# Optimization experiments

Hardware: AMD Instinct MI355X
Metric: run time of the kernel (lower is better)

Reference implementation:

```python
import jax, jax.numpy as jnp
import numpy as np

B, C1, C2, K, S, HDIM = 8, 16, 16, 3, 1, 16
H = W = 64


def setup_inputs() -> dict:
    key = jax.random.key(0)
    k0, k1, k2 = jax.random.split(key, 3)
    x = jax.random.normal(k0, (B, C1, H, W), jnp.float32)
    # torch.nn.Linear default init scale ~ 1/sqrt(fan_in)
    fc1_w = jax.random.normal(k1, (HDIM, 5), jnp.float32) * (1.0 / np.sqrt(5.0))
    fc1_b = jnp.zeros((HDIM,), jnp.float32)
    fc2_w = jax.random.normal(k2, (C2 * C1 * K * K, HDIM), jnp.float32) * (1.0 / np.sqrt(HDIM))
    fc2_b = jnp.zeros((C2 * C1 * K * K,), jnp.float32)
    return {"x": x, "fc1_w": fc1_w, "fc1_b": fc1_b, "fc2_w": fc2_w, "fc2_b": fc2_b}


def _unfold_same(x, k, s):
    """F.pad('same'-style) + F.unfold. Returns (patches [B, L, C*k*k], out_h, out_w).
    Channel ordering matches torch unfold: index = c*k*k + i*k + j (channel-major)."""
    Bq, C, Hq, Wq = x.shape
    out_h = (Hq + s - 1) // s
    out_w = (Wq + s - 1) // s
    pad_h = max((out_h - 1) * s + k - Hq, 0)
    pad_w = max((out_w - 1) * s + k - Wq, 0)
    pt, pb = pad_h // 2, pad_h - pad_h // 2
    pl, pr = pad_w // 2, pad_w - pad_w // 2
    xp = jnp.pad(x, ((0, 0), (0, 0), (pt, pb), (pl, pr)))
    # k*k shifted views; loop over tiny fixed k*k=9 taps only
    cols = jnp.stack(
        [xp[:, :, i:i + out_h * s:s, j:j + out_w * s:s] for i in range(k) for j in range(k)],
        axis=2,
    )  # [B, C, k*k, out_h, out_w]
    patches = cols.reshape(Bq, C * k * k, out_h * out_w).transpose(0, 2, 1)  # [B, L, C*k*k]
    return patches, out_h, out_w


def reference(x, fc1_w, fc1_b, fc2_w, fc2_b):
    patches, oh, ow = _unfold_same(x, K, S)  # [B, L, N] with N = C1*K*K
    Bq, L, N = patches.shape
    mu = patches.mean(-1, keepdims=True)
    # torch.std default is unbiased (ddof=1)
    var = jnp.sum((patches - mu) ** 2, axis=-1, keepdims=True) / (N - 1)
    sigma = jnp.sqrt(var) + 1e-6
    normed = (patches - mu) / sigma
    skew = jnp.mean(normed ** 3, axis=-1, keepdims=True)
    kurt = jnp.mean(normed ** 4, axis=-1, keepdims=True) - 3.0
    prob = jax.nn.softmax(patches, axis=-1)
    entropy = -jnp.sum(prob * jnp.log(prob + 1e-6), axis=-1, keepdims=True)
    stats = jnp.concatenate([mu, sigma, skew, kurt, entropy], axis=-1)  # [B, L, 5]
    stats = jax.lax.stop_gradient(stats)  # .detach() in the original
    h = jax.nn.relu(stats @ fc1_w.T + fc1_b)                 # [B, L, hdim]
    weights = (h @ fc2_w.T + fc2_b).reshape(Bq, L, C2, N)    # [B, L, c2, c1*k*k]
    out = jnp.einsum('blco,blo->blc', weights, patches)      # per-location dynamic conv
    return out.transpose(0, 2, 1).reshape(Bq, C2, oh, ow)
```

## Files before the change

### kernel.cpp

```cpp
#include <hip/hip_runtime.h>
#include <math.h>


typedef __attribute__((ext_vector_type(8))) short short8;
typedef __attribute__((ext_vector_type(4))) float float4v;

#define NPq 144
#define QSTR 280

__device__ __forceinline__ unsigned short f2bf(float f) {
    unsigned int u = __builtin_bit_cast(unsigned int, f);
    u += 0x7fffu + ((u >> 16) & 1u);
    return (unsigned short)(u >> 16);
}
__device__ __forceinline__ float bf2f(unsigned short h) {
    unsigned int u = ((unsigned int)h) << 16;
    return __builtin_bit_cast(float, u);
}

__global__ void prep_bfrag(const float* __restrict__ fc2_w,
                           const float* __restrict__ fc2_b,
                           unsigned short* __restrict__ Bfrag) {
    const int blk  = blockIdx.x;
    const int t    = blk / 5, s = blk % 5;
    const int lane = threadIdx.x;
    const int n    = lane & 15, q = lane >> 4;
    short8 v;
#pragma unroll
    for (int j = 0; j < 8; ++j) {
        const int k = s * 32 + q * 8 + j;
        float w = 0.f;
        if (k < NPq) w = (t < 16) ? fc2_w[(t * NPq + k) * 16 + n]
                                  : fc2_b[n * NPq + k];
        v[j] = (short)f2bf(w);
    }
    *(short8*)(Bfrag + (size_t)(blk * 64 + lane) * 8) = v;
}

__global__ __launch_bounds__(256, 2) void sacconv_kernel(
    const float* __restrict__ x,
    const float* __restrict__ fc1_w,
    const float* __restrict__ fc1_b,
    const unsigned short* __restrict__ Bfrag,
    float* __restrict__ out)
{
    __shared__ unsigned short SA[4 * 5 * 64 * 8];
    __shared__ __attribute__((aligned(16))) unsigned short Qs[64 * QSTR];
    __shared__ float Hl[64][20];

    const int t   = threadIdx.x;
    const int blk = blockIdx.x;
    const int b   = blk >> 6;
    const int y   = blk & 63;

    const int lane = t & 63;
    const int w    = __builtin_amdgcn_readfirstlane(t >> 6);
    const int m    = lane & 15;
    const int q    = lane >> 4;
    const int loc  = w * 16 + m;

    float* XsG = (float*)Qs;
    float* Xs  = XsG + 4;

    const short8* Bf = (const short8*)Bfrag;
    short8 bb0[5], bb1[5], bb2[5];
#pragma unroll
    for (int s = 0; s < 5; ++s) bb0[s] = Bf[(w * 5 + s) * 64 + lane];

    {
        const float4 z4 = make_float4(0.f, 0.f, 0.f, 0.f);
        if (t < 48) *(float4*)&Xs[t * 68 + 64] = z4;
        if (t == 48) *(float4*)&XsG[0] = z4;
        const int ybad = (y == 0) ? 0 : ((y == 63) ? 2 : -1);
        if (ybad >= 0) {
#pragma unroll
            for (int u = 0; u < 2; ++u) {
                const int idx = t + 256 * u;
                if (idx < 272) {
                    const int ch = idx / 17, sg = idx % 17;
                    *(float4*)&Xs[ch * 204 + ybad * 68 + sg * 4] = z4;
                }
            }
        }
#pragma unroll
        for (int u = 0; u < 3; ++u) {
            const int idx = t + 256 * u;
            const int r  = idx >> 4, sg = idx & 15;
            const int ch = r / 3;
            const int dy = r - ch * 3;
            const int yy = y + dy - 1;
            if (yy >= 0 && yy < 64) {
                const float4 d = *(const float4*)&x[(((b * 16 + ch) * 64 + yy) << 6) + sg * 4];
                *(float4*)&Xs[r * 68 + sg * 4] = d;
            }
        }
    }
    __syncthreads();

    float v[36];
    float sum = 0.f, mx = -1e30f;
    {
        const float* basep = &Xs[q * 816 + loc - 1];
#pragma unroll
        for (int i = 0; i < 36; ++i) {
            const int g  = i / 9;
            const int r9 = i % 9;
            const int ii = r9 / 3, jj = r9 % 3;
            const float val = basep[g * 204 + ii * 68 + jj];
            v[i] = val;
            sum += val;
            mx  = fmaxf(mx, val);
        }
    }

    {
        unsigned int pk[18];
#pragma unroll
        for (int p = 0; p < 18; ++p)
            pk[p] = (unsigned int)f2bf(v[2 * p]) | ((unsigned int)f2bf(v[2 * p + 1]) << 16);
        const int g0 = (36 * q) >> 3;
        auto hwa = [&](int g) { return ((w * 5 + (g >> 2)) * 64 + (g & 3) * 16 + m) * 8; };
        if ((q & 1) == 0) {
#pragma unroll
            for (int u = 0; u < 4; ++u)
                *(uint4*)&SA[hwa(g0 + u)] = make_uint4(pk[4*u], pk[4*u+1], pk[4*u+2], pk[4*u+3]);
            *(uint2*)&SA[hwa(g0 + 4)] = make_uint2(pk[16], pk[17]);
        } else {
            *(uint2*)&SA[hwa(g0) + 4] = make_uint2(pk[0], pk[1]);
#pragma unroll
            for (int u = 0; u < 4; ++u)
                *(uint4*)&SA[hwa(g0 + 1 + u)] = make_uint4(pk[4*u+2], pk[4*u+3], pk[4*u+4], pk[4*u+5]);
        }
        if (lane < 32)
            *(uint4*)&SA[((w * 5 + 4) * 64 + 32 + lane) * 8] = make_uint4(0u, 0u, 0u, 0u);
    }

    sum += __shfl_xor(sum, 16, 64);
    sum += __shfl_xor(sum, 32, 64);
    mx = fmaxf(mx, __shfl_xor(mx, 16, 64));
    mx = fmaxf(mx, __shfl_xor(mx, 32, 64));
    const float mu = sum * (1.f / 144.f);

    float m2 = 0.f, m3 = 0.f, m4 = 0.f, se = 0.f, sev = 0.f;
#pragma unroll
    for (int i = 0; i < 36; ++i) {
        const float d  = v[i] - mu;
        const float d2 = d * d;
        m2 += d2; m3 += d2 * d; m4 += d2 * d2;
        const float e = __expf(v[i] - mx);
        se += e; sev += e * v[i];
    }
    m2 += __shfl_xor(m2, 16, 64);  m2 += __shfl_xor(m2, 32, 64);
    m3 += __shfl_xor(m3, 16, 64);  m3 += __shfl_xor(m3, 32, 64);
    m4 += __shfl_xor(m4, 16, 64);  m4 += __shfl_xor(m4, 32, 64);
    se += __shfl_xor(se, 16, 64);  se += __shfl_xor(se, 32, 64);
    sev += __shfl_xor(sev, 16, 64); sev += __shfl_xor(sev, 32, 64);

    const float var   = m2 * (1.f / 143.f);
    const float sigma = sqrtf(var) + 1e-6f;
    const float is    = 1.f / sigma;
    const float is2   = is * is;
    const float skew  = (m3 * (1.f / 144.f)) * is2 * is;
    const float kurt  = (m4 * (1.f / 144.f)) * is2 * is2 - 3.f;
    const float ent   = __logf(se) + mx - sev / se;

    {
        float h4[4];
#pragma unroll
        for (int j0 = 0; j0 < 4; ++j0) {
            const int j = q * 4 + j0;
            const float* wr = fc1_w + j * 5;
            const float hv = mu * wr[0] + sigma * wr[1] + skew * wr[2]
                           + kurt * wr[3] + ent * wr[4] + fc1_b[j];
            h4[j0] = fmaxf(hv, 0.f);
        }
        *(float4*)&Hl[loc][q * 4] = make_float4(h4[0], h4[1], h4[2], h4[3]);
    }

#pragma unroll
    for (int s = 0; s < 5; ++s) bb1[s] = Bf[((w + 4) * 5 + s) * 64 + lane];

    __syncthreads();

    short8 af[4][5];
#pragma unroll
    for (int mm = 0; mm < 4; ++mm)
#pragma unroll
        for (int s = 0; s < 5; ++s)
            af[mm][s] = *(const short8*)&SA[((mm * 5 + s) * 64 + lane) * 8];

    float4v acc[4][4];
#pragma unroll
    for (int u = 0; u < 4; ++u)
#pragma unroll
        for (int mm = 0; mm < 4; ++mm) acc[u][mm] = (float4v){0.f, 0.f, 0.f, 0.f};
    float4v acc4[4];
#pragma unroll
    for (int mm = 0; mm < 4; ++mm) acc4[mm] = (float4v){0.f, 0.f, 0.f, 0.f};

#pragma unroll
    for (int s = 0; s < 5; ++s) bb2[s] = Bf[((w + 8) * 5 + s) * 64 + lane];
#pragma unroll
    for (int mm = 0; mm < 4; ++mm)
#pragma unroll
        for (int s = 0; s < 5; ++s)
            acc[0][mm] = __builtin_amdgcn_mfma_f32_16x16x32_bf16(af[mm][s], bb0[s], acc[0][mm], 0, 0, 0);

#pragma unroll
    for (int s = 0; s < 5; ++s) bb0[s] = Bf[((w + 12) * 5 + s) * 64 + lane];
#pragma unroll
    for (int mm = 0; mm < 4; ++mm)
#pragma unroll
        for (int s = 0; s < 5; ++s)
            acc[1][mm] = __builtin_amdgcn_mfma_f32_16x16x32_bf16(af[mm][s], bb1[s], acc[1][mm], 0, 0, 0);

    if (w == 3) {
#pragma unroll
        for (int s = 0; s < 5; ++s) bb1[s] = Bf[(16 * 5 + s) * 64 + lane];
    }
#pragma unroll
    for (int mm = 0; mm < 4; ++mm)
#pragma unroll
        for (int s = 0; s < 5; ++s)
            acc[2][mm] = __builtin_amdgcn_mfma_f32_16x16x32_bf16(af[mm][s], bb2[s], acc[2][mm], 0, 0, 0);

#pragma unroll
    for (int mm = 0; mm < 4; ++mm)
#pragma unroll
        for (int s = 0; s < 5; ++s)
            acc[3][mm] = __builtin_amdgcn_mfma_f32_16x16x32_bf16(af[mm][s], bb0[s], acc[3][mm], 0, 0, 0);

    if (w == 3) {
#pragma unroll
        for (int mm = 0; mm < 4; ++mm)
#pragma unroll
            for (int s = 0; s < 5; ++s)
                acc4[mm] = __builtin_amdgcn_mfma_f32_16x16x32_bf16(af[mm][s], bb1[s], acc4[mm], 0, 0, 0);
    }

    {
        const int nn = lane & 15, qq = lane >> 4;
#pragma unroll
        for (int u = 0; u < 4; ++u) {
            const int col = (w + 4 * u) * 16 + nn;
#pragma unroll
            for (int mm = 0; mm < 4; ++mm) {
                const int rowb = mm * 16 + qq * 4;
#pragma unroll
                for (int r = 0; r < 4; ++r)
                    Qs[(rowb + r) * QSTR + col] = f2bf(acc[u][mm][r]);
            }
        }
        if (w == 3) {
#pragma unroll
            for (int mm = 0; mm < 4; ++mm) {
                const int rowb = mm * 16 + qq * 4;
#pragma unroll
                for (int r = 0; r < 4; ++r)
                    Qs[(rowb + r) * QSTR + 256 + nn] = f2bf(acc4[mm][r]);
            }
        }
    }
    __syncthreads();

    {
        float hv[16];
#pragma unroll
        for (int j = 0; j < 16; ++j) hv[j] = Hl[lane][j];
        const int cg = w * 4;
#pragma unroll
        for (int cc = 0; cc < 4; ++cc) {
            const int c = cg + cc;
            const unsigned short* qr = &Qs[lane * QSTR + c * 16];
            short8 q0 = *(const short8*)qr;
            short8 q1 = *(const short8*)(qr + 8);
            float res = bf2f(Qs[lane * QSTR + 256 + c]);
#pragma unroll
            for (int j = 0; j < 8; ++j) res += hv[j]     * bf2f((unsigned short)q0[j]);
#pragma unroll
            for (int j = 0; j < 8; ++j) res += hv[8 + j] * bf2f((unsigned short)q1[j]);
            out[(b * 16 + c) * 4096 + y * 64 + lane] = res;
        }
    }
}

extern "C" void kernel_launch(void* const* d_in, const int* in_sizes, int n_in,
                              void* d_out, int out_size, void* d_ws, size_t ws_size,
                              hipStream_t stream) {
    const float* x     = (const float*)d_in[0];
    const float* fc1_w = (const float*)d_in[1];
    const float* fc1_b = (const float*)d_in[2];
    const float* fc2_w = (const float*)d_in[3];
    const float* fc2_b = (const float*)d_in[4];
    float* out = (float*)d_out;
    unsigned short* Bfrag = (unsigned short*)d_ws;

    prep_bfrag<<<85, 64, 0, stream>>>(fc2_w, fc2_b, Bfrag);
    sacconv_kernel<<<512, 256, 0, stream>>>(x, fc1_w, fc1_b, Bfrag, out);
}
```

Baseline: 70.69 us.

## Fuse weight-fragment prep into main kernel with flag-based cross-block sync

Removes the separate prep_bfrag launch. The first 85 blocks of the main kernel now build the bf16 B fragments, staging fc2_w through shared memory so the global reads are coalesced. Each of those blocks then publishes a release flag, and every block spin-waits on all 85 flags before loading the fragments. The Hl hidden-activation buffer is also transposed. The flags are never reset, so calls after the first can read Bfrag while it is being rewritten. This only works because the values are identical each time, and it relies on all blocks being co-resident.

Result: slower. 103.0 us (+45.7%).

```diff
diff --git a/kernel.cpp b/kernel.cpp
--- a/kernel.cpp
+++ b/kernel.cpp
@@ -7,6 +7,7 @@
 
 #define NPq 144
 #define QSTR 280
+#define MAGICF 0x13572468u
 
 __device__ __forceinline__ unsigned short f2bf(float f) {
     unsigned int u = __builtin_bit_cast(unsigned int, f);
@@ -18,35 +19,19 @@
     return __builtin_bit_cast(float, u);
 }
 
-__global__ void prep_bfrag(const float* __restrict__ fc2_w,
-                           const float* __restrict__ fc2_b,
-                           unsigned short* __restrict__ Bfrag) {
-    const int blk  = blockIdx.x;
-    const int t    = blk / 5, s = blk % 5;
-    const int lane = threadIdx.x;
-    const int n    = lane & 15, q = lane >> 4;
-    short8 v;
-#pragma unroll
-    for (int j = 0; j < 8; ++j) {
-        const int k = s * 32 + q * 8 + j;
-        float w = 0.f;
-        if (k < NPq) w = (t < 16) ? fc2_w[(t * NPq + k) * 16 + n]
-                                  : fc2_b[n * NPq + k];
-        v[j] = (short)f2bf(w);
-    }
-    *(short8*)(Bfrag + (size_t)(blk * 64 + lane) * 8) = v;
-}
-
 __global__ __launch_bounds__(256, 2) void sacconv_kernel(
     const float* __restrict__ x,
     const float* __restrict__ fc1_w,
     const float* __restrict__ fc1_b,
-    const unsigned short* __restrict__ Bfrag,
+    const float* __restrict__ fc2_w,
+    const float* __restrict__ fc2_b,
+    unsigned short* Bfrag,
+    unsigned int*   flags,
     float* __restrict__ out)
 {
     __shared__ unsigned short SA[4 * 5 * 64 * 8];
     __shared__ __attribute__((aligned(16))) unsigned short Qs[64 * QSTR];
-    __shared__ float Hl[64][20];
+    __shared__ float Hl[16 * 68];
 
     const int t   = threadIdx.x;
     const int blk = blockIdx.x;
@@ -59,13 +44,56 @@
     const int q    = lane >> 4;
     const int loc  = w * 16 + m;
 
+    if (blk < 85) {
+        const int tt = blk / 5, ss = blk % 5;
+        if (tt < 16) {
+            float* Td = (float*)SA;
+            if (t < 128) {
+                const int rr = t >> 2, cs = t & 3;
+                const int k  = ss * 32 + rr;
+                float4 d = make_float4(0.f, 0.f, 0.f, 0.f);
+                if (k < NPq) d = *(const float4*)&fc2_w[(tt * NPq + k) * 16 + cs * 4];
+                Td[rr * 17 + cs * 4 + 0] = d.x;
+                Td[rr * 17 + cs * 4 + 1] = d.y;
+                Td[rr * 17 + cs * 4 + 2] = d.z;
+                Td[rr * 17 + cs * 4 + 3] = d.w;
+            }
+            __syncthreads();
+            if (t < 64) {
+                const int n = t & 15, qq = t >> 4;
+                short8 v;
+#pragma unroll
+                for (int j = 0; j < 8; ++j)
+                    v[j] = (short)f2bf(Td[(qq * 8 + j) * 17 + n]);
+                *(short8*)(Bfrag + (size_t)(blk * 64 + t) * 8) = v;
+            }
+        } else {
+            if (t < 64) {
+                const int n = t & 15, qq = t >> 4;
+                const int kb = ss * 32 + qq * 8;
+                float4 d0 = make_float4(0.f, 0.f, 0.f, 0.f), d1 = d0;
+                if (kb < NPq) {
+                    d0 = *(const float4*)&fc2_b[n * NPq + kb];
+                    d1 = *(const float4*)&fc2_b[n * NPq + kb + 4];
+                }
+                short8 v;
+                v[0] = (short)f2bf(d0.x); v[1] = (short)f2bf(d0.y);
+                v[2] = (short)f2bf(d0.z); v[3] = (short)f2bf(d0.w);
+                v[4] = (short)f2bf(d1.x); v[5] = (short)f2bf(d1.y);
+                v[6] = (short)f2bf(d1.z); v[7] = (short)f2bf(d1.w);
+                *(short8*)(Bfrag + (size_t)(blk * 64 + t) * 8) = v;
+            }
+        }
+        __syncthreads();
+        if (t == 0) {
+            __threadfence();
+            __hip_atomic_store(&flags[blk], MAGICF, __ATOMIC_RELEASE,
+                               __HIP_MEMORY_SCOPE_AGENT);
+        }
+    }
+
     float* XsG = (float*)Qs;
     float* Xs  = XsG + 4;
-
-    const short8* Bf = (const short8*)Bfrag;
-    short8 bb0[5], bb1[5], bb2[5];
-#pragma unroll
-    for (int s = 0; s < 5; ++s) bb0[s] = Bf[(w * 5 + s) * 64 + lane];
 
     {
         const float4 z4 = make_float4(0.f, 0.f, 0.f, 0.f);
@@ -165,22 +193,30 @@
     const float ent   = __logf(se) + mx - sev / se;
 
     {
-        float h4[4];
 #pragma unroll
         for (int j0 = 0; j0 < 4; ++j0) {
             const int j = q * 4 + j0;
             const float* wr = fc1_w + j * 5;
             const float hv = mu * wr[0] + sigma * wr[1] + skew * wr[2]
                            + kurt * wr[3] + ent * wr[4] + fc1_b[j];
-            h4[j0] = fmaxf(hv, 0.f);
-        }
-        *(float4*)&Hl[loc][q * 4] = make_float4(h4[0], h4[1], h4[2], h4[3]);
-    }
-
+            Hl[j * 68 + loc] = fmaxf(hv, 0.f);
+        }
+    }
+
+    if (t < 85) {
+        while (__hip_atomic_load(&flags[t], __ATOMIC_RELAXED,
+                                 __HIP_MEMORY_SCOPE_AGENT) != MAGICF)
+            __builtin_amdgcn_s_sleep(1);
+    }
+    __threadfence();
+    __syncthreads();
+
+    const short8* Bf = (const short8*)Bfrag;
+    short8 bb0[5], bb1[5], bb2[5];
+#pragma unroll
+    for (int s = 0; s < 5; ++s) bb0[s] = Bf[(w * 5 + s) * 64 + lane];
 #pragma unroll
     for (int s = 0; s < 5; ++s) bb1[s] = Bf[((w + 4) * 5 + s) * 64 + lane];
-
-    __syncthreads();
 
     short8 af[4][5];
 #pragma unroll
@@ -266,7 +302,7 @@
     {
         float hv[16];
 #pragma unroll
-        for (int j = 0; j < 16; ++j) hv[j] = Hl[lane][j];
+        for (int j = 0; j < 16; ++j) hv[j] = Hl[j * 68 + lane];
         const int cg = w * 4;
 #pragma unroll
         for (int cc = 0; cc < 4; ++cc) {
@@ -294,7 +330,8 @@
     const float* fc2_b = (const float*)d_in[4];
     float* out = (float*)d_out;
     unsigned short* Bfrag = (unsigned short*)d_ws;
-
-    prep_bfrag<<<85, 64, 0, stream>>>(fc2_w, fc2_b, Bfrag);
-    sacconv_kernel<<<512, 256, 0, stream>>>(x, fc1_w, fc1_b, Bfrag, out);
+    unsigned int*   flags = (unsigned int*)((char*)d_ws + 87296);
+
+    sacconv_kernel<<<512, 256, 0, stream>>>(x, fc1_w, fc1_b, fc2_w, fc2_b,
+                                            Bfrag, flags, out);
 }
```
